# Kernel tuning notes

Hardware: AMD Instinct MI355X
Metric: run time of the kernel (lower is better)

## Reference

```python
import jax, jax.numpy as jnp
import numpy as np

SMOOTHING = 0.05
CONFIDENCE = 1.0 - SMOOTHING
B, C = 32768, 2048


def setup_inputs() -> dict:
    key = jax.random.key(0)
    k1, k2, k3 = jax.random.split(key, 3)
    x = jax.random.normal(k1, (B, C), dtype=jnp.float32)
    target = jax.random.randint(k2, (B,), 0, C, dtype=jnp.int64)
    class_loss_weight = jax.random.uniform(k3, (C,), dtype=jnp.float32)
    return {"x": x, "target": target, "class_loss_weight": class_loss_weight}


def reference(x, target, class_loss_weight):
    # logprobs: [B, C]
    logprobs = jax.nn.log_softmax(x, axis=-1)
    # nll_loss: [B] = -logprobs[i, target[i]]
    nll_loss = -jnp.take_along_axis(logprobs, target[:, None], axis=-1)[:, 0]
    # smooth_loss: [B] = -mean over classes
    smooth_loss = -jnp.mean(logprobs, axis=-1)
    # per-sample class weights (vectorized replacement for the python loop)
    w = class_loss_weight[target]  # [B]
    w_sum = jnp.sum(w)
    loss = CONFIDENCE * nll_loss * w + SMOOTHING * smooth_loss
    return jnp.sum(loss) / w_sum
```

## Files before the change

### kernel.cpp

```cpp
#include <hip/hip_runtime.h>
#include <math.h>

#define SMOOTHING_F   0.05f
#define CONFIDENCE_F  0.95f
#define C_DIM         2048
#define WPB           4
#define GRID_BLOCKS   1024

struct Row {
    float4 v[8];
    float  wt, xt;
};

__device__ __forceinline__ void load_row(const float* __restrict__ x,
                                         const int*   __restrict__ target,
                                         const float* __restrict__ cw,
                                         int row, int lane, Row& r) {
    const float4* xr = (const float4*)(x + (size_t)row * C_DIM);
#pragma unroll
    for (int k = 0; k < 8; ++k) r.v[k] = xr[lane + 64 * k];
    const int t = target[row];
    r.wt = cw[t];
    r.xt = x[(size_t)row * C_DIM + t];
}

__device__ __forceinline__ void process_row(const Row& r, int lane,
                                            double& loss_acc, double& w_acc) {
    float se = 0.0f, sx = 0.0f;
#pragma unroll
    for (int k = 0; k < 8; ++k) {
        se += __expf(r.v[k].x) + __expf(r.v[k].y)
            + __expf(r.v[k].z) + __expf(r.v[k].w);
        sx += (r.v[k].x + r.v[k].y) + (r.v[k].z + r.v[k].w);
    }
#pragma unroll
    for (int off = 32; off > 0; off >>= 1) {
        se += __shfl_xor(se, off, 64);
        sx += __shfl_xor(sx, off, 64);
    }
    if (lane == 0) {
        const float lse    = __logf(se);
        const float nll    = lse - r.xt;
        const float smooth = lse - sx * (1.0f / C_DIM);
        loss_acc += (double)(CONFIDENCE_F * nll * r.wt + SMOOTHING_F * smooth);
        w_acc    += (double)r.wt;
    }
}

__global__ __launch_bounds__(256, 4) void ls_main(
    const float* __restrict__ x,
    const int*   __restrict__ target,
    const float* __restrict__ cw,
    double*      __restrict__ ws,
    int B)
{
    const int lane   = threadIdx.x & 63;
    const int wave   = threadIdx.x >> 6;
    const int stride = gridDim.x * WPB;

    double loss_acc = 0.0, w_acc = 0.0;

    int row = blockIdx.x * WPB + wave;

    Row A, Bb;
    if (row < B) load_row(x, target, cw, row, lane, A);

    while (row < B) {
        int next = row + stride;
        if (next < B) load_row(x, target, cw, next, lane, Bb);
        process_row(A, lane, loss_acc, w_acc);
        row = next;
        if (row >= B) break;

        next = row + stride;
        if (next < B) load_row(x, target, cw, next, lane, A);
        process_row(Bb, lane, loss_acc, w_acc);
        row = next;
    }

    __shared__ double s_loss[WPB];
    __shared__ double s_w[WPB];
    if (lane == 0) { s_loss[wave] = loss_acc; s_w[wave] = w_acc; }
    __syncthreads();
    if (threadIdx.x == 0) {
        double L = 0.0, W = 0.0;
#pragma unroll
        for (int i = 0; i < WPB; ++i) { L += s_loss[i]; W += s_w[i]; }
        ws[2 * blockIdx.x]     = L;
        ws[2 * blockIdx.x + 1] = W;
    }
}

__global__ __launch_bounds__(256) void ls_reduce(
    const double* __restrict__ ws, float* __restrict__ out, int nPartials)
{
    const int tid  = threadIdx.x;
    const int lane = tid & 63;
    const int wave = tid >> 6;

    double L = 0.0, W = 0.0;
    for (int i = tid; i < nPartials; i += 256) {
        L += ws[2 * i];
        W += ws[2 * i + 1];
    }
#pragma unroll
    for (int off = 32; off > 0; off >>= 1) {
        L += __shfl_xor(L, off, 64);
        W += __shfl_xor(W, off, 64);
    }
    __shared__ double sL[4], sW[4];
    if (lane == 0) { sL[wave] = L; sW[wave] = W; }
    __syncthreads();
    if (tid == 0) {
        out[0] = (float)((sL[0] + sL[1] + sL[2] + sL[3]) /
                         (sW[0] + sW[1] + sW[2] + sW[3]));
    }
}

extern "C" void kernel_launch(void* const* d_in, const int* in_sizes, int n_in,
                              void* d_out, int out_size, void* d_ws, size_t ws_size,
                              hipStream_t stream) {
    const float* x      = (const float*)d_in[0];
    const int*   target = (const int*)  d_in[1];
    const float* cw     = (const float*)d_in[2];
    float*       out    = (float*)d_out;
    double*      ws     = (double*)d_ws;

    const int B = in_sizes[1];

    ls_main<<<GRID_BLOCKS, 64 * WPB, 0, stream>>>(x, target, cw, ws, B);
    ls_reduce<<<1, 256, 0, stream>>>(ws, out, GRID_BLOCKS);
}
```

Before: 359.0 us.

## Defer row-sum reduction to end, prefetch targets a row ahead, split exp accumulators

Each lane now keeps a running sum of x and subtracts its scaled total from the loss once at the end, which removes one wave shuffle-reduction per row. Target indices are loaded one row further ahead, so the dependent gathers for the class weight and the target logit no longer wait on a fresh target load. The exp sums are spread over four independent accumulators to shorten the dependency chain. The kernel is likely memory-bound, so the gain may be small. Float accumulation of sx across many rows could lose some precision.

New measurement: 358.6 us. No clear change (-0.1%).

```diff
diff --git a/kernel.cpp b/kernel.cpp
--- a/kernel.cpp
+++ b/kernel.cpp
@@ -7,42 +7,41 @@
 #define WPB           4
 #define GRID_BLOCKS   1024
 
-struct Row {
+struct RowData {
     float4 v[8];
     float  wt, xt;
 };
 
-__device__ __forceinline__ void load_row(const float* __restrict__ x,
-                                         const int*   __restrict__ target,
-                                         const float* __restrict__ cw,
-                                         int row, int lane, Row& r) {
+__device__ __forceinline__ void issue_row(const float* __restrict__ x,
+                                          const float* __restrict__ cw,
+                                          int row, int t, int lane, RowData& r) {
     const float4* xr = (const float4*)(x + (size_t)row * C_DIM);
 #pragma unroll
     for (int k = 0; k < 8; ++k) r.v[k] = xr[lane + 64 * k];
-    const int t = target[row];
     r.wt = cw[t];
     r.xt = x[(size_t)row * C_DIM + t];
 }
 
-__device__ __forceinline__ void process_row(const Row& r, int lane,
+__device__ __forceinline__ void process_row(const RowData& r, int lane,
+                                            float& sx_lane,
                                             double& loss_acc, double& w_acc) {
-    float se = 0.0f, sx = 0.0f;
+    float se0 = 0.f, se1 = 0.f, se2 = 0.f, se3 = 0.f;
 #pragma unroll
     for (int k = 0; k < 8; ++k) {
-        se += __expf(r.v[k].x) + __expf(r.v[k].y)
-            + __expf(r.v[k].z) + __expf(r.v[k].w);
-        sx += (r.v[k].x + r.v[k].y) + (r.v[k].z + r.v[k].w);
+        se0 += __expf(r.v[k].x);
+        se1 += __expf(r.v[k].y);
+        se2 += __expf(r.v[k].z);
+        se3 += __expf(r.v[k].w);
+        sx_lane += (r.v[k].x + r.v[k].y) + (r.v[k].z + r.v[k].w);
     }
+    float se = (se0 + se1) + (se2 + se3);
 #pragma unroll
-    for (int off = 32; off > 0; off >>= 1) {
+    for (int off = 32; off > 0; off >>= 1)
         se += __shfl_xor(se, off, 64);
-        sx += __shfl_xor(sx, off, 64);
-    }
     if (lane == 0) {
-        const float lse    = __logf(se);
-        const float nll    = lse - r.xt;
-        const float smooth = lse - sx * (1.0f / C_DIM);
-        loss_acc += (double)(CONFIDENCE_F * nll * r.wt + SMOOTHING_F * smooth);
+        const float lse = __logf(se);
+        loss_acc += (double)(CONFIDENCE_F * (lse - r.xt) * r.wt
+                             + SMOOTHING_F * lse);
         w_acc    += (double)r.wt;
     }
 }
@@ -59,24 +58,39 @@
     const int stride = gridDim.x * WPB;
 
     double loss_acc = 0.0, w_acc = 0.0;
+    float  sx_lane  = 0.0f;
 
     int row = blockIdx.x * WPB + wave;
 
-    Row A, Bb;
-    if (row < B) load_row(x, target, cw, row, lane, A);
+    RowData A, Bf;
+    int tB = 0;
+    if (row < B) {
+        const int tA = target[row];
+        issue_row(x, cw, row, tA, lane, A);
+        const int r1 = row + stride;
+        if (r1 < B) tB = target[r1];
+    }
 
     while (row < B) {
-        int next = row + stride;
-        if (next < B) load_row(x, target, cw, next, lane, Bb);
-        process_row(A, lane, loss_acc, w_acc);
-        row = next;
+        int n1 = row + stride, n2 = n1 + stride;
+        if (n1 < B) issue_row(x, cw, n1, tB, lane, Bf);
+        int tC = (n2 < B) ? target[n2] : 0;
+        process_row(A, lane, sx_lane, loss_acc, w_acc);
+        tB = tC; row = n1;
         if (row >= B) break;
 
-        next = row + stride;
-        if (next < B) load_row(x, target, cw, next, lane, A);
-        process_row(Bb, lane, loss_acc, w_acc);
-        row = next;
+        n1 = row + stride; n2 = n1 + stride;
+        if (n1 < B) issue_row(x, cw, n1, tB, lane, A);
+        tC = (n2 < B) ? target[n2] : 0;
+        process_row(Bf, lane, sx_lane, loss_acc, w_acc);
+        tB = tC; row = n1;
     }
+
+#pragma unroll
+    for (int off = 32; off > 0; off >>= 1)
+        sx_lane += __shfl_xor(sx_lane, off, 64);
+    if (lane == 0)
+        loss_acc -= (double)(SMOOTHING_F * sx_lane * (1.0f / C_DIM));
 
     __shared__ double s_loss[WPB];
     __shared__ double s_w[WPB];
```
